# Kernel tuning notes

Measured on AMD Instinct MI355X. Metric: run time of the kernel, lower is better.

## Reference

```python
import jax, jax.numpy as jnp
import numpy as np
from jax import lax

BN_EPS = 1e-5


def _condconv(x, w, b, fc_w, fc_b):
    """CondConv2D: per-sample expert mixing then 3x3 conv (pad=1, stride=1).
    x: [B, Cin, H, W]; w: [E, Cout, Cin, 3, 3]; b: [Cout]; fc_w: [E, Cin]; fc_b: [E].
    """
    B, Cin, H, W = x.shape
    E, Cout, _, kh, kw = w.shape
    pooled = x.mean(axis=(2, 3))                               # [B, Cin] adaptive_avg_pool2d(1,1)+flatten
    rw = jax.nn.sigmoid(pooled @ fc_w.T + fc_b)                # [B, E] routing weights
    kernels = jnp.einsum('be,eoihw->boihw', rw, w)             # [B, Cout, Cin, 3, 3]
    # Batched per-sample conv via grouped conv: groups = B
    xi = x.reshape(1, B * Cin, H, W)
    ker = kernels.reshape(B * Cout, Cin, kh, kw)
    out = lax.conv_general_dilated(
        xi, ker, window_strides=(1, 1), padding=((1, 1), (1, 1)),
        feature_group_count=B,
        dimension_numbers=('NCHW', 'OIHW', 'NCHW'))
    return out.reshape(B, Cout, H, W) + b[None, :, None, None]


def _bn_relu(x, g, b, m, v):
    # eval-mode BatchNorm2d followed by ReLU
    inv = g * lax.rsqrt(v + BN_EPS)
    return jax.nn.relu(x * inv[None, :, None, None] + (b - m * inv)[None, :, None, None])


def setup_inputs() -> dict:
    key = jax.random.key(0)
    ks = jax.random.split(key, 8)
    B, Cin, Cout, H, W, E = 16, 64, 128, 128, 128, 3
    s1 = 1.0 / np.sqrt(Cin * 9)
    s2 = 1.0 / np.sqrt(Cout * 9)
    return {
        'x': jax.random.normal(ks[0], (B, Cin, H, W), jnp.float32),
        'w1': jax.random.normal(ks[1], (E, Cout, Cin, 3, 3), jnp.float32) * s1,
        'b1': jax.random.normal(ks[2], (Cout,), jnp.float32) * s1,
        'fc1_w': jax.random.normal(ks[3], (E, Cin), jnp.float32) / np.sqrt(Cin),
        'fc1_b': jnp.zeros((E,), jnp.float32),
        'bn1_g': jnp.ones((Cout,), jnp.float32),
        'bn1_b': jnp.zeros((Cout,), jnp.float32),
        'bn1_m': jnp.zeros((Cout,), jnp.float32),
        'bn1_v': jnp.ones((Cout,), jnp.float32),
        'w2': jax.random.normal(ks[4], (E, Cout, Cout, 3, 3), jnp.float32) * s2,
        'b2': jax.random.normal(ks[5], (Cout,), jnp.float32) * s2,
        'fc2_w': jax.random.normal(ks[6], (E, Cout), jnp.float32) / np.sqrt(Cout),
        'fc2_b': jnp.zeros((E,), jnp.float32),
        'bn2_g': jnp.ones((Cout,), jnp.float32),
        'bn2_b': jnp.zeros((Cout,), jnp.float32),
        'bn2_m': jnp.zeros((Cout,), jnp.float32),
        'bn2_v': jnp.ones((Cout,), jnp.float32),
    }


def reference(x, w1, b1, fc1_w, fc1_b, bn1_g, bn1_b, bn1_m, bn1_v,
              w2, b2, fc2_w, fc2_b, bn2_g, bn2_b, bn2_m, bn2_v):
    h = _condconv(x, w1, b1, fc1_w, fc1_b)
    h = _bn_relu(h, bn1_g, bn1_b, bn1_m, bn1_v)
    h = _condconv(h, w2, b2, fc2_w, fc2_b)
    h = _bn_relu(h, bn2_g, bn2_b, bn2_m, bn2_v)
    return h
```

## Files before the change

### kernel.cpp

```cpp
#include <hip/hip_runtime.h>
#include <math.h>

#define BN_EPS 1e-5f

typedef short bf16x8 __attribute__((ext_vector_type(8)));
typedef float f32x4 __attribute__((ext_vector_type(4)));
typedef float f32x16 __attribute__((ext_vector_type(16)));
typedef unsigned short ushort8v __attribute__((ext_vector_type(8)));
typedef unsigned int uint;
typedef unsigned short ushort;

__device__ inline ushort f2bf(float f) {
    uint u = __float_as_uint(f);
    uint r = u + 0x7FFFu + ((u >> 16) & 1u);
    return (ushort)(r >> 16);
}
__device__ inline float bf2f(ushort u) { return __uint_as_float(((uint)u) << 16); }
__device__ inline uint cvtpk(float lo, float hi) {
    uint r;
    asm("v_cvt_pk_bf16_f32 %0, %1, %2" : "=v"(r) : "v"(lo), "v"(hi));
    return r;
}

__global__ void scsh_kernel(const float* b1, const float* g1, const float* bb1,
                            const float* m1, const float* v1,
                            const float* b2, const float* g2, const float* bb2,
                            const float* m2, const float* v2,
                            float* scsh1, float* scsh2) {
    int t = threadIdx.x;
    if (t < 128) {
        float sc = g1[t] * rsqrtf(v1[t] + BN_EPS);
        scsh1[t] = sc;
        scsh1[128 + t] = (b1[t] - m1[t]) * sc + bb1[t];
    } else {
        int c = t - 128;
        float sc = g2[c] * rsqrtf(v2[c] + BN_EPS);
        scsh2[c] = sc;
        scsh2[128 + c] = (b2[c] - m2[c]) * sc + bb2[c];
    }
}

__global__ void xprep_kernel(const float* __restrict__ x, ushort* __restrict__ xT,
                             float* __restrict__ pooled1) {
    __shared__ float t[64][65];
    const int b = blockIdx.y;
    const int p0 = blockIdx.x * 64;
    const int tid = threadIdx.x;
#pragma unroll
    for (int it = 0; it < 16; ++it) {
        const int idx = it * 256 + tid;
        const int ci = idx >> 6, p = idx & 63;
        t[ci][p] = x[((size_t)b * 64 + ci) * 16384 + p0 + p];
    }
    __syncthreads();
    const int h = p0 >> 7;
#pragma unroll
    for (int it = 0; it < 2; ++it) {
        const int p = it * 32 + (tid >> 3);
        const int w = (p0 & 127) + p;
        const int c0 = (tid & 7) * 8;
        const int cc = c0 >> 4;
        ushort8v u;
#pragma unroll
        for (int j = 0; j < 8; ++j) u[j] = f2bf(t[c0 + j][p]);
        *(ushort8v*)&xT[(((size_t)(b * 128 + h) * 4 + cc) * 128 + w) * 16 + (c0 & 15)] = u;
    }
    if (tid < 64) {
        float s = 0.f;
#pragma unroll 8
        for (int p = 0; p < 64; ++p) s += t[tid][p];
        atomicAdd(&pooled1[b * 64 + tid], s);
    }
}

__global__ void pool2h_kernel(const ushort* __restrict__ hT, float* __restrict__ pooled2) {
    const int b = blockIdx.x, slab = blockIdx.y;
    const int tid = threadIdx.x;
    const int cc = tid >> 5, o = (tid >> 4) & 1, wb = tid & 15;
    float a[8] = {0.f, 0.f, 0.f, 0.f, 0.f, 0.f, 0.f, 0.f};
    for (int r = 0; r < 4; ++r) {
        const int h = slab * 4 + r;
        const ushort* base = hT + ((size_t)(b * 128 + h) * 8 + cc) * 2048 + o * 8;
#pragma unroll
        for (int k = 0; k < 8; ++k) {
            const ushort8v u = *(const ushort8v*)(base + (wb + k * 16) * 16);
#pragma unroll
            for (int j = 0; j < 8; ++j) a[j] += bf2f(u[j]);
        }
    }
    __shared__ float sp[16][8][17];
    const int grp0 = cc * 2 + o;
#pragma unroll
    for (int j = 0; j < 8; ++j) sp[grp0][j][wb] = a[j];
    __syncthreads();
    if (tid < 128) {
        const int grp = tid >> 3, j = tid & 7;
        float s = 0.f;
#pragma unroll
        for (int k = 0; k < 16; ++k) s += sp[grp][j][k];
        const int c = (grp >> 1) * 16 + (grp & 1) * 8 + j;
        atomicAdd(&pooled2[b * 128 + c], s);
    }
}

template <int CIN>
__global__ void mix_route_kernel(const float* __restrict__ w, const float* __restrict__ pooled,
                                 const float* __restrict__ fcw, const float* __restrict__ fcb,
                                 ushort* __restrict__ wmix) {
    constexpr int NCC = CIN / 16;
    __shared__ float rwl[48];
    const int tid = threadIdx.x;
    if (tid < 48) {
        const int bb = tid / 3, e = tid % 3;
        float d = 0.f;
        for (int c = 0; c < CIN; ++c) d += pooled[bb * CIN + c] * fcw[e * CIN + c];
        const float s = fcb[e] + d * (1.f / 16384.f);
        rwl[tid] = 1.f / (1.f + expf(-s));
    }
    __syncthreads();
    const int co = blockIdx.x;
    for (int b = 0; b < 16; ++b) {
        const float r0 = rwl[b * 3 + 0], r1 = rwl[b * 3 + 1], r2 = rwl[b * 3 + 2];
        for (int idx = tid; idx < CIN * 9; idx += 256) {
            const int ci = idx & (CIN - 1);
            const int tap = idx / CIN;
            const size_t off = ((size_t)co * CIN + ci) * 9 + tap;
            const float m = r0 * w[off]
                          + r1 * w[off + (size_t)128 * CIN * 9]
                          + r2 * w[off + (size_t)2 * 128 * CIN * 9];
            const int cc = ci >> 4, o = (ci >> 3) & 1, e = ci & 7;
            const size_t dst = ((size_t)(b * NCC + cc) * 2304
                             + tap * 256 + o * 128 + co) * 8 + e;
            wmix[dst] = f2bf(m);
        }
    }
}

template <int CIN, bool TO_BF16>
__global__ __launch_bounds__(1024, 4)
void conv_mfma9_kernel(const ushort* __restrict__ xT, const ushort* __restrict__ wmix,
                       const float* __restrict__ scsh,
                       float* __restrict__ outf, ushort* __restrict__ outh) {
    constexpr int NCC = CIN / 16;
    constexpr int IBUF = 24960;
    constexpr int WOFF = 2 * IBUF;
    constexpr int WBUF = 36864;
    __shared__ __align__(16) char smem[123648];

    const int L = ((blockIdx.x & 7) << 6) | (blockIdx.x >> 3);
    const int b = L >> 5;
    const int rt = L & 31;

    const int tid = threadIdx.x;
    const int lane = tid & 63, wid = tid >> 6;
    const int wm = wid >> 3;
    const int wn8 = wid & 7;
    const int prow = wn8 >> 1;
    const int pcb = (wn8 & 1) * 64;
    const int l31 = lane & 31, lhi = lane >> 5;

    f32x16 acc[2][2];
#pragma unroll
    for (int i = 0; i < 2; ++i)
#pragma unroll
        for (int j = 0; j < 2; ++j)
#pragma unroll
            for (int r = 0; r < 16; ++r) acc[i][j][r] = 0.f;

    const ushort* inb = xT + (size_t)b * 128 * NCC * 2048;
    const ushort* wmb = wmix + (size_t)b * NCC * 18432;

    const int ihalf = wid & 1, ioct = (wid >> 1) & 1, ir0 = (wid & 15) >> 2;
    const int iv = (ihalf * 64 + lane) * 16 + ioct * 8;
    const int idst0 = (ir0 * 260 + ioct * 130 + 1 + ihalf * 64) * 16;
    const int hg0 = rt * 4 - 1 + ir0;
    const int wo0 = wid * 512 + lane * 8;
    const int wd0 = wid * 1024 + lane * 16;

    auto stage = [&](char* dI, char* dW, int cc) {
        const size_t ccI = (size_t)cc * 2048;
        {
            const int hg = hg0;
            if ((unsigned)hg < 128u) {
                const ushort* src = inb + (size_t)hg * (NCC * 2048) + ccI + iv;
                __builtin_amdgcn_global_load_lds(
                    (const __attribute__((address_space(1))) void*)src,
                    (__attribute__((address_space(3))) void*)(dI + idst0),
                    16, 0, 0);
            }
        }
        if (wid < 8) {
            const int hg = hg0 + 4;
            if ((unsigned)hg < 128u) {
                const ushort* src = inb + (size_t)hg * (NCC * 2048) + ccI + iv;
                __builtin_amdgcn_global_load_lds(
                    (const __attribute__((address_space(1))) void*)src,
                    (__attribute__((address_space(3))) void*)(dI + idst0 + 4 * 4160),
                    16, 0, 0);
            }
        }
        const ushort* ws = wmb + (size_t)cc * 18432;
#pragma unroll
        for (int u = 0; u < 2; ++u) {
            __builtin_amdgcn_global_load_lds(
                (const __attribute__((address_space(1))) void*)(ws + wo0 + u * 8192),
                (__attribute__((address_space(3))) void*)(dW + wd0 + u * 16384),
                16, 0, 0);
        }
        if (wid < 4) {
            __builtin_amdgcn_global_load_lds(
                (const __attribute__((address_space(1))) void*)(ws + wo0 + 16384),
                (__attribute__((address_space(3))) void*)(dW + wd0 + 32768),
                16, 0, 0);
        }
    };

    const int ibase = (prow * 260 + lhi * 130 + pcb + l31) * 16;
    const int wbase = (lhi * 128 + wm * 64 + l31) * 16;
    const char* pI0 = smem + ibase;
    const char* pI1 = smem + IBUF + ibase;
    const char* pW0 = smem + WOFF + wbase;
    const char* pW1 = smem + WOFF + WBUF + wbase;

    auto taps = [&](const char* ldsI, const char* ldsW) {
#pragma unroll
        for (int tap = 0; tap < 9; ++tap) {
            const int dy = tap / 3, dx = tap - dy * 3;
            bf16x8 af[2];
#pragma unroll
            for (int mf = 0; mf < 2; ++mf)
                af[mf] = *(const bf16x8*)(ldsW + (tap * 4096 + mf * 512));
#pragma unroll
            for (int nf = 0; nf < 2; ++nf) {
                const bf16x8 bv = *(const bf16x8*)(ldsI + (dy * 4160 + nf * 512 + dx * 16));
#pragma unroll
                for (int mf = 0; mf < 2; ++mf)
                    acc[mf][nf] = __builtin_amdgcn_mfma_f32_32x32x16_bf16(
                        af[mf], bv, acc[mf][nf], 0, 0, 0);
            }
        }
    };

    if (tid < 48) {
        const int bi = tid >= 24, idx = tid - bi * 24;
        const int r = idx >> 2, j = idx & 3;
        const int g = r * 260 + (j >> 1) * 130 + (j & 1) * 129;
        *(f32x4*)(smem + bi * IBUF + g * 16) = f32x4{0.f, 0.f, 0.f, 0.f};
    }
    if (rt == 0 || rt == 31) {
        const int r = (rt == 0) ? 0 : 5;
        if (tid < 520) {
            const int bi = tid >= 260, gr = tid - bi * 260;
            *(f32x4*)(smem + bi * IBUF + (r * 260 + gr) * 16) = f32x4{0.f, 0.f, 0.f, 0.f};
        }
    }

    stage(smem, smem + WOFF, 0);
    asm volatile("s_waitcnt vmcnt(0)" ::: "memory");
    __syncthreads();

    for (int cc = 0; cc < NCC; cc += 2) {
        stage(smem + IBUF, smem + WOFF + WBUF, cc + 1);
        __builtin_amdgcn_sched_barrier(0);
        taps(pI0, pW0);
        __syncthreads();
        if (cc + 2 < NCC) stage(smem, smem + WOFF, cc + 2);
        __builtin_amdgcn_sched_barrier(0);
        taps(pI1, pW1);
        __syncthreads();
    }

    if constexpr (!TO_BF16) {
#pragma unroll
        for (int mf = 0; mf < 2; ++mf) {
            const int cob = wm * 64 + mf * 32 + 4 * lhi;
            f32x4 sc[4], sh[4];
#pragma unroll
            for (int q = 0; q < 4; ++q) {
                sc[q] = *(const f32x4*)&scsh[cob + 8 * q];
                sh[q] = *(const f32x4*)&scsh[128 + cob + 8 * q];
            }
#pragma unroll
            for (int nf = 0; nf < 2; ++nf) {
                const size_t pbase = (size_t)(rt * 4 + prow) * 128 + pcb + nf * 32 + l31;
#pragma unroll
                for (int q = 0; q < 4; ++q)
#pragma unroll
                    for (int s = 0; s < 4; ++s) {
                        float y = fmaf(acc[mf][nf][q * 4 + s], sc[q][s], sh[q][s]);
                        y = y > 0.f ? y : 0.f;
                        outf[((size_t)(b * 128 + cob + 8 * q + s)) * 16384 + pbase] = y;
                    }
            }
        }
    } else {
        ushort* sf = (ushort*)smem;
#pragma unroll
        for (int p = 0; p < 2; ++p) {
            if ((prow >> 1) == p) {
                const int lr = prow & 1;
#pragma unroll
                for (int mf = 0; mf < 2; ++mf)
#pragma unroll
                    for (int q = 0; q < 4; ++q) {
                        const int co4 = wm * 64 + mf * 32 + 8 * q + 4 * lhi;
                        const f32x4 sc = *(const f32x4*)&scsh[co4];
                        const f32x4 sh = *(const f32x4*)&scsh[128 + co4];
#pragma unroll
                        for (int nf = 0; nf < 2; ++nf) {
                            const int px = lr * 128 + pcb + nf * 32 + l31;
                            float v[4];
#pragma unroll
                            for (int s = 0; s < 4; ++s) {
                                float y = fmaf(acc[mf][nf][q * 4 + s], sc[s], sh[s]);
                                v[s] = y > 0.f ? y : 0.f;
                            }
                            uint2 pk;
                            pk.x = cvtpk(v[0], v[1]);
                            pk.y = cvtpk(v[2], v[3]);
                            *(uint2*)&sf[px * 136 + co4] = pk;
                        }
                    }
            }
            __syncthreads();
#pragma unroll
            for (int it = 0; it < 2; ++it) {
                const int id = it * 1024 + tid;
                const int lr = id >> 10, cc = (id >> 7) & 7, w = id & 127;
                const uint4 v0 = *(const uint4*)&sf[(lr * 128 + w) * 136 + cc * 16];
                const uint4 v1 = *(const uint4*)&sf[(lr * 128 + w) * 136 + cc * 16 + 8];
                ushort* dst = outh + (((size_t)(b * 128 + rt * 4 + 2 * p + lr)) * 8 + cc) * 2048 + w * 16;
                *(uint4*)dst = v0;
                *(uint4*)(dst + 8) = v1;
            }
            if (p == 0) __syncthreads();
        }
    }
}

extern "C" void kernel_launch(void* const* d_in, const int* in_sizes, int n_in,
                              void* d_out, int out_size, void* d_ws, size_t ws_size,
                              hipStream_t stream) {
    const float* x     = (const float*)d_in[0];
    const float* w1    = (const float*)d_in[1];
    const float* b1    = (const float*)d_in[2];
    const float* fc1_w = (const float*)d_in[3];
    const float* fc1_b = (const float*)d_in[4];
    const float* bn1g  = (const float*)d_in[5];
    const float* bn1b  = (const float*)d_in[6];
    const float* bn1m  = (const float*)d_in[7];
    const float* bn1v  = (const float*)d_in[8];
    const float* w2    = (const float*)d_in[9];
    const float* b2    = (const float*)d_in[10];
    const float* fc2_w = (const float*)d_in[11];
    const float* fc2_b = (const float*)d_in[12];
    const float* bn2g  = (const float*)d_in[13];
    const float* bn2b  = (const float*)d_in[14];
    const float* bn2m  = (const float*)d_in[15];
    const float* bn2v  = (const float*)d_in[16];

    float* out = (float*)d_out;
    char* ws = (char*)d_ws;

    ushort* hT    = (ushort*)(ws + 0);
    ushort* xT    = (ushort*)(ws + 67108864);
    ushort* wmix1 = (ushort*)(ws + 100663296);
    ushort* wmix2 = (ushort*)(ws + 103022592);
    float*  pool1 = (float*) (ws + 107741184);
    float*  pool2 = (float*) (ws + 107745280);
    float*  scsh1 = (float*) (ws + 107753472);
    float*  scsh2 = (float*) (ws + 107754496);

    hipMemsetAsync(pool1, 0, 4096, stream);
    hipMemsetAsync(pool2, 0, 8192, stream);

    scsh_kernel<<<1, 256, 0, stream>>>(b1, bn1g, bn1b, bn1m, bn1v,
                                       b2, bn2g, bn2b, bn2m, bn2v, scsh1, scsh2);

    xprep_kernel<<<dim3(256, 16), 256, 0, stream>>>(x, xT, pool1);
    mix_route_kernel<64><<<128, 256, 0, stream>>>(w1, pool1, fc1_w, fc1_b, wmix1);
    conv_mfma9_kernel<64, true><<<512, 1024, 0, stream>>>(
        xT, wmix1, scsh1, nullptr, hT);

    pool2h_kernel<<<dim3(16, 32), 256, 0, stream>>>(hT, pool2);
    mix_route_kernel<128><<<128, 256, 0, stream>>>(w2, pool2, fc2_w, fc2_b, wmix2);
    conv_mfma9_kernel<128, false><<<512, 1024, 0, stream>>>(
        hT, wmix2, scsh2, out, nullptr);
}
```

Baseline: 203.5 us.

## Load mixed weights directly from global into registers instead of LDS staging

The conv kernel no longer stages the per-sample mixed weights through shared memory. Each wave reads its A fragments straight from global memory (likely L2-resident), prefetching the first two taps ahead of the input staging. This cuts LDS use from about 124KB to about 70KB and removes the weight copy and LDS reads. The cost is global-load latency inside the tap loop and redundant weight reads across waves.

```diff
diff --git a/kernel.cpp b/kernel.cpp
--- a/kernel.cpp
+++ b/kernel.cpp
@@ -138,14 +138,12 @@
 
 template <int CIN, bool TO_BF16>
 __global__ __launch_bounds__(1024, 4)
-void conv_mfma9_kernel(const ushort* __restrict__ xT, const ushort* __restrict__ wmix,
-                       const float* __restrict__ scsh,
-                       float* __restrict__ outf, ushort* __restrict__ outh) {
+void conv_mfma10_kernel(const ushort* __restrict__ xT, const ushort* __restrict__ wmix,
+                        const float* __restrict__ scsh,
+                        float* __restrict__ outf, ushort* __restrict__ outh) {
     constexpr int NCC = CIN / 16;
     constexpr int IBUF = 24960;
-    constexpr int WOFF = 2 * IBUF;
-    constexpr int WBUF = 36864;
-    __shared__ __align__(16) char smem[123648];
+    __shared__ __align__(16) char smem[69632];
 
     const int L = ((blockIdx.x & 7) << 6) | (blockIdx.x >> 3);
     const int b = L >> 5;
@@ -168,26 +166,22 @@
             for (int r = 0; r < 16; ++r) acc[i][j][r] = 0.f;
 
     const ushort* inb = xT + (size_t)b * 128 * NCC * 2048;
-    const ushort* wmb = wmix + (size_t)b * NCC * 18432;
+    const ushort* wmb = wmix + (size_t)b * NCC * 18432
+                      + lhi * 1024 + wm * 512 + l31 * 8;
 
     const int ihalf = wid & 1, ioct = (wid >> 1) & 1, ir0 = (wid & 15) >> 2;
     const int iv = (ihalf * 64 + lane) * 16 + ioct * 8;
     const int idst0 = (ir0 * 260 + ioct * 130 + 1 + ihalf * 64) * 16;
     const int hg0 = rt * 4 - 1 + ir0;
-    const int wo0 = wid * 512 + lane * 8;
-    const int wd0 = wid * 1024 + lane * 16;
-
-    auto stage = [&](char* dI, char* dW, int cc) {
+
+    auto stage = [&](char* dI, int cc) {
         const size_t ccI = (size_t)cc * 2048;
-        {
-            const int hg = hg0;
-            if ((unsigned)hg < 128u) {
-                const ushort* src = inb + (size_t)hg * (NCC * 2048) + ccI + iv;
-                __builtin_amdgcn_global_load_lds(
-                    (const __attribute__((address_space(1))) void*)src,
-                    (__attribute__((address_space(3))) void*)(dI + idst0),
-                    16, 0, 0);
-            }
+        if ((unsigned)hg0 < 128u) {
+            const ushort* src = inb + (size_t)hg0 * (NCC * 2048) + ccI + iv;
+            __builtin_amdgcn_global_load_lds(
+                (const __attribute__((address_space(1))) void*)src,
+                (__attribute__((address_space(3))) void*)(dI + idst0),
+                16, 0, 0);
         }
         if (wid < 8) {
             const int hg = hg0 + 4;
@@ -199,40 +193,38 @@
                     16, 0, 0);
             }
         }
-        const ushort* ws = wmb + (size_t)cc * 18432;
-#pragma unroll
-        for (int u = 0; u < 2; ++u) {
-            __builtin_amdgcn_global_load_lds(
-                (const __attribute__((address_space(1))) void*)(ws + wo0 + u * 8192),
-                (__attribute__((address_space(3))) void*)(dW + wd0 + u * 16384),
-                16, 0, 0);
-        }
-        if (wid < 4) {
-            __builtin_amdgcn_global_load_lds(
-                (const __attribute__((address_space(1))) void*)(ws + wo0 + 16384),
-                (__attribute__((address_space(3))) void*)(dW + wd0 + 32768),
-                16, 0, 0);
-        }
     };
 
     const int ibase = (prow * 260 + lhi * 130 + pcb + l31) * 16;
-    const int wbase = (lhi * 128 + wm * 64 + l31) * 16;
     const char* pI0 = smem + ibase;
     const char* pI1 = smem + IBUF + ibase;
-    const char* pW0 = smem + WOFF + wbase;
-    const char* pW1 = smem + WOFF + WBUF + wbase;
-
-    auto taps = [&](const char* ldsI, const char* ldsW) {
+
+    auto chunkFn = [&](const char* pI, char* dN, int cc, bool st) {
+        const ushort* wcc = wmb + (size_t)cc * 18432;
+        bf16x8 afp[2][2];
+#pragma unroll
+        for (int t = 0; t < 2; ++t)
+#pragma unroll
+            for (int mf = 0; mf < 2; ++mf)
+                afp[t][mf] = *(const bf16x8*)(wcc + t * 2048 + mf * 256);
+        __builtin_amdgcn_sched_barrier(0);
+        if (st) stage(dN, cc + 1);
+        __builtin_amdgcn_sched_barrier(0);
 #pragma unroll
         for (int tap = 0; tap < 9; ++tap) {
             const int dy = tap / 3, dx = tap - dy * 3;
             bf16x8 af[2];
-#pragma unroll
-            for (int mf = 0; mf < 2; ++mf)
-                af[mf] = *(const bf16x8*)(ldsW + (tap * 4096 + mf * 512));
+            if (tap < 2) {
+                af[0] = afp[tap][0];
+                af[1] = afp[tap][1];
+            } else {
+#pragma unroll
+                for (int mf = 0; mf < 2; ++mf)
+                    af[mf] = *(const bf16x8*)(wcc + tap * 2048 + mf * 256);
+            }
 #pragma unroll
             for (int nf = 0; nf < 2; ++nf) {
-                const bf16x8 bv = *(const bf16x8*)(ldsI + (dy * 4160 + nf * 512 + dx * 16));
+                const bf16x8 bv = *(const bf16x8*)(pI + (dy * 4160 + nf * 512 + dx * 16));
 #pragma unroll
                 for (int mf = 0; mf < 2; ++mf)
                     acc[mf][nf] = __builtin_amdgcn_mfma_f32_32x32x16_bf16(
@@ -255,18 +247,14 @@
         }
     }
 
-    stage(smem, smem + WOFF, 0);
+    stage(smem, 0);
     asm volatile("s_waitcnt vmcnt(0)" ::: "memory");
     __syncthreads();
 
     for (int cc = 0; cc < NCC; cc += 2) {
-        stage(smem + IBUF, smem + WOFF + WBUF, cc + 1);
-        __builtin_amdgcn_sched_barrier(0);
-        taps(pI0, pW0);
+        chunkFn(pI0, smem + IBUF, cc, true);
         __syncthreads();
-        if (cc + 2 < NCC) stage(smem, smem + WOFF, cc + 2);
-        __builtin_amdgcn_sched_barrier(0);
-        taps(pI1, pW1);
+        chunkFn(pI1, smem, cc + 1, cc + 2 < NCC);
         __syncthreads();
     }
 
@@ -379,11 +367,11 @@
 
     xprep_kernel<<<dim3(256, 16), 256, 0, stream>>>(x, xT, pool1);
     mix_route_kernel<64><<<128, 256, 0, stream>>>(w1, pool1, fc1_w, fc1_b, wmix1);
-    conv_mfma9_kernel<64, true><<<512, 1024, 0, stream>>>(
+    conv_mfma10_kernel<64, true><<<512, 1024, 0, stream>>>(
         xT, wmix1, scsh1, nullptr, hT);
 
     pool2h_kernel<<<dim3(16, 32), 256, 0, stream>>>(hT, pool2);
     mix_route_kernel<128><<<128, 256, 0, stream>>>(w2, pool2, fc2_w, fc2_b, wmix2);
-    conv_mfma9_kernel<128, false><<<512, 1024, 0, stream>>>(
+    conv_mfma10_kernel<128, false><<<512, 1024, 0, stream>>>(
         hT, wmix2, scsh2, out, nullptr);
 }
```

New measurement: 215.3 us. 5.8% more time.

## Remap conv wave tiles to two rows and reuse input fragments across dy taps

Applied to the files above, without the earlier changes.

Each wave now covers two adjacent output rows of one 32-pixel column block, where it previously covered one row of 64 pixels. Input B-fragments for the three dx offsets are kept in registers and slid down between dy steps. This cuts LDS reads of the input tile from 18 to 12 per channel chunk per wave. In exchange it uses more registers for the held fragments and changes the LDS access pattern, which could add bank conflicts or register pressure under the 1024-thread launch bounds.

```diff
diff --git a/kernel.cpp b/kernel.cpp
--- a/kernel.cpp
+++ b/kernel.cpp
@@ -138,9 +138,9 @@
 
 template <int CIN, bool TO_BF16>
 __global__ __launch_bounds__(1024, 4)
-void conv_mfma9_kernel(const ushort* __restrict__ xT, const ushort* __restrict__ wmix,
-                       const float* __restrict__ scsh,
-                       float* __restrict__ outf, ushort* __restrict__ outh) {
+void conv_mfma11_kernel(const ushort* __restrict__ xT, const ushort* __restrict__ wmix,
+                        const float* __restrict__ scsh,
+                        float* __restrict__ outf, ushort* __restrict__ outh) {
     constexpr int NCC = CIN / 16;
     constexpr int IBUF = 24960;
     constexpr int WOFF = 2 * IBUF;
@@ -154,9 +154,8 @@
     const int tid = threadIdx.x;
     const int lane = tid & 63, wid = tid >> 6;
     const int wm = wid >> 3;
-    const int wn8 = wid & 7;
-    const int prow = wn8 >> 1;
-    const int pcb = (wn8 & 1) * 64;
+    const int rp = (wid >> 2) & 1;
+    const int cb = wid & 3;
     const int l31 = lane & 31, lhi = lane >> 5;
 
     f32x16 acc[2][2];
@@ -179,15 +178,12 @@
 
     auto stage = [&](char* dI, char* dW, int cc) {
         const size_t ccI = (size_t)cc * 2048;
-        {
-            const int hg = hg0;
-            if ((unsigned)hg < 128u) {
-                const ushort* src = inb + (size_t)hg * (NCC * 2048) + ccI + iv;
-                __builtin_amdgcn_global_load_lds(
-                    (const __attribute__((address_space(1))) void*)src,
-                    (__attribute__((address_space(3))) void*)(dI + idst0),
-                    16, 0, 0);
-            }
+        if ((unsigned)hg0 < 128u) {
+            const ushort* src = inb + (size_t)hg0 * (NCC * 2048) + ccI + iv;
+            __builtin_amdgcn_global_load_lds(
+                (const __attribute__((address_space(1))) void*)src,
+                (__attribute__((address_space(3))) void*)(dI + idst0),
+                16, 0, 0);
         }
         if (wid < 8) {
             const int hg = hg0 + 4;
@@ -215,28 +211,38 @@
         }
     };
 
-    const int ibase = (prow * 260 + lhi * 130 + pcb + l31) * 16;
+    const int ibase = (rp * 2 * 260 + lhi * 130 + cb * 32 + l31) * 16;
     const int wbase = (lhi * 128 + wm * 64 + l31) * 16;
     const char* pI0 = smem + ibase;
     const char* pI1 = smem + IBUF + ibase;
     const char* pW0 = smem + WOFF + wbase;
     const char* pW1 = smem + WOFF + WBUF + wbase;
 
-    auto taps = [&](const char* ldsI, const char* ldsW) {
-#pragma unroll
-        for (int tap = 0; tap < 9; ++tap) {
-            const int dy = tap / 3, dx = tap - dy * 3;
-            bf16x8 af[2];
-#pragma unroll
-            for (int mf = 0; mf < 2; ++mf)
-                af[mf] = *(const bf16x8*)(ldsW + (tap * 4096 + mf * 512));
-#pragma unroll
-            for (int nf = 0; nf < 2; ++nf) {
-                const bf16x8 bv = *(const bf16x8*)(ldsI + (dy * 4160 + nf * 512 + dx * 16));
-#pragma unroll
-                for (int mf = 0; mf < 2; ++mf)
-                    acc[mf][nf] = __builtin_amdgcn_mfma_f32_32x32x16_bf16(
-                        af[mf], bv, acc[mf][nf], 0, 0, 0);
+    auto taps = [&](const char* pI, const char* pW) {
+        bf16x8 rb0[3], rb1[3];
+#pragma unroll
+        for (int dx = 0; dx < 3; ++dx) {
+            rb0[dx] = *(const bf16x8*)(pI + (0 * 260 + dx) * 16);
+            rb1[dx] = *(const bf16x8*)(pI + (1 * 260 + dx) * 16);
+        }
+#pragma unroll
+        for (int dy = 0; dy < 3; ++dy) {
+#pragma unroll
+            for (int dx = 0; dx < 3; ++dx) {
+                const int tap = dy * 3 + dx;
+                const bf16x8 af0 = *(const bf16x8*)(pW + (tap * 256) * 16);
+                const bf16x8 af1 = *(const bf16x8*)(pW + (tap * 256 + 32) * 16);
+                acc[0][0] = __builtin_amdgcn_mfma_f32_32x32x16_bf16(af0, rb0[dx], acc[0][0], 0, 0, 0);
+                acc[1][0] = __builtin_amdgcn_mfma_f32_32x32x16_bf16(af1, rb0[dx], acc[1][0], 0, 0, 0);
+                acc[0][1] = __builtin_amdgcn_mfma_f32_32x32x16_bf16(af0, rb1[dx], acc[0][1], 0, 0, 0);
+                acc[1][1] = __builtin_amdgcn_mfma_f32_32x32x16_bf16(af1, rb1[dx], acc[1][1], 0, 0, 0);
+            }
+            if (dy < 2) {
+#pragma unroll
+                for (int dx = 0; dx < 3; ++dx) {
+                    rb0[dx] = rb1[dx];
+                    rb1[dx] = *(const bf16x8*)(pI + ((dy + 2) * 260 + dx) * 16);
+                }
             }
         }
     };
@@ -282,7 +288,7 @@
             }
 #pragma unroll
             for (int nf = 0; nf < 2; ++nf) {
-                const size_t pbase = (size_t)(rt * 4 + prow) * 128 + pcb + nf * 32 + l31;
+                const size_t pbase = (size_t)(rt * 4 + rp * 2 + nf) * 128 + cb * 32 + l31;
 #pragma unroll
                 for (int q = 0; q < 4; ++q)
 #pragma unroll
@@ -297,8 +303,7 @@
         ushort* sf = (ushort*)smem;
 #pragma unroll
         for (int p = 0; p < 2; ++p) {
-            if ((prow >> 1) == p) {
-                const int lr = prow & 1;
+            if (rp == p) {
 #pragma unroll
                 for (int mf = 0; mf < 2; ++mf)
 #pragma unroll
@@ -308,7 +313,7 @@
                         const f32x4 sh = *(const f32x4*)&scsh[128 + co4];
 #pragma unroll
                         for (int nf = 0; nf < 2; ++nf) {
-                            const int px = lr * 128 + pcb + nf * 32 + l31;
+                            const int px = nf * 128 + cb * 32 + l31;
                             float v[4];
 #pragma unroll
                             for (int s = 0; s < 4; ++s) {
@@ -379,11 +384,11 @@
 
     xprep_kernel<<<dim3(256, 16), 256, 0, stream>>>(x, xT, pool1);
     mix_route_kernel<64><<<128, 256, 0, stream>>>(w1, pool1, fc1_w, fc1_b, wmix1);
-    conv_mfma9_kernel<64, true><<<512, 1024, 0, stream>>>(
+    conv_mfma11_kernel<64, true><<<512, 1024, 0, stream>>>(
         xT, wmix1, scsh1, nullptr, hT);
 
     pool2h_kernel<<<dim3(16, 32), 256, 0, stream>>>(hT, pool2);
     mix_route_kernel<128><<<128, 256, 0, stream>>>(w2, pool2, fc2_w, fc2_b, wmix2);
-    conv_mfma9_kernel<128, false><<<512, 1024, 0, stream>>>(
+    conv_mfma11_kernel<128, false><<<512, 1024, 0, stream>>>(
         hT, wmix2, scsh2, out, nullptr);
 }
```

New measurement: 204.1 us. Within noise of the previous version (+0.3%).
